# Optimization experiments

Measured on AMD Instinct MI355X. Metric: run time of the kernel, lower is better.

The kernel has to match this reference:

```python
import jax, jax.numpy as jnp
import numpy as np

N = 50000
E = 800000
N_IN = 256
N_HID = 128
N_OUT = 64
HOP = 10


def setup_inputs() -> dict:
    key = jax.random.key(0)
    ks = jax.random.split(key, 12)
    x = jax.random.normal(ks[0], (N, N_IN), dtype=jnp.float32)
    s = jax.random.randint(ks[1], (E,), 0, N, dtype=jnp.int32)
    t = jax.random.randint(ks[2], (E,), 0, N, dtype=jnp.int32)
    # parameters (xavier-ish scaling)
    fc1W = jax.random.normal(ks[3], (N_HID, N_IN), dtype=jnp.float32) * (1.0 / np.sqrt(N_IN))
    fc1b = jnp.zeros((N_HID,), dtype=jnp.float32)
    fcsW = jax.random.normal(ks[4], (HOP, N_HID, N_HID), dtype=jnp.float32) * (1.0 / np.sqrt(N_HID))
    fcsb = jnp.zeros((HOP, N_HID), dtype=jnp.float32)
    a1 = jax.random.normal(ks[5], (HOP, N_HID), dtype=jnp.float32) * (1.0 / np.sqrt(N_HID))
    a2 = jax.random.normal(ks[6], (HOP, N_HID), dtype=jnp.float32) * (1.0 / np.sqrt(N_HID))
    fc2W = jax.random.normal(ks[7], (N_OUT, N_HID), dtype=jnp.float32) * (1.0 / np.sqrt(N_HID))
    fc2b = jnp.zeros((N_OUT,), dtype=jnp.float32)
    return {"x": x, "s": s, "t": t, "fc1W": fc1W, "fc1b": fc1b,
            "fcsW": fcsW, "fcsb": fcsb, "a1": a1, "a2": a2,
            "fc2W": fc2W, "fc2b": fc2b}


def reference(x, s, t, fc1W, fc1b, fcsW, fcsb, a1, a2, fc2W, fc2b):
    # dropout layers are identity in eval mode
    x = jax.nn.relu(x @ fc1W.T + fc1b)  # [N, n_hid]
    h = x
    for i in range(HOP):
        W, b = fcsW[i], fcsb[i]
        x_new = x @ W.T + b          # [N, n_hid]
        h = h @ W.T + b              # [N, n_hid]
        x1 = x_new @ a1[i]           # [N]
        h1 = h @ a2[i]               # [N]
        w1 = jnp.exp(jax.nn.leaky_relu(x1[s] + h1[t], 0.2))       # [E]
        w2 = jnp.exp(jax.nn.leaky_relu(x1 + x_new @ a2[i], 0.2))  # [N]
        div = jax.ops.segment_sum(w1, s, num_segments=N) + w2     # [N]
        num = jax.ops.segment_sum(w1[:, None] * h[t], s, num_segments=N) + w2[:, None] * x_new
        h = jax.nn.elu(num / div[:, None])
    return h @ fc2W.T + fc2b  # [N, n_out]
```

## Files before the change

### kernel.cpp

```cpp
#include <hip/hip_runtime.h>
#include <math.h>


typedef __attribute__((ext_vector_type(8))) short short8;
typedef __attribute__((ext_vector_type(4))) float f32x4;
#define MFMA16 __builtin_amdgcn_mfma_f32_16x16x32_bf16

__device__ __forceinline__ float lrelu02(float v) { return v > 0.f ? v : 0.2f * v; }

__device__ __forceinline__ float2 bf2f2(unsigned int v) {
    return make_float2(__uint_as_float(v << 16), __uint_as_float(v & 0xffff0000u));
}
__device__ __forceinline__ unsigned int f2bf(float f) {
    unsigned int u = __float_as_uint(f);
    u += 0x7fffu + ((u >> 16) & 1u);
    return u >> 16;
}
__device__ __forceinline__ float hi_part(float f) {
    return __uint_as_float(__float_as_uint(f) & 0xffff0000u);
}
__device__ __forceinline__ uint4 pack_hi(const float4& a, const float4& b) {
    uint4 r;
    r.x = (__float_as_uint(a.x) >> 16) | (__float_as_uint(a.y) & 0xffff0000u);
    r.y = (__float_as_uint(a.z) >> 16) | (__float_as_uint(a.w) & 0xffff0000u);
    r.z = (__float_as_uint(b.x) >> 16) | (__float_as_uint(b.y) & 0xffff0000u);
    r.w = (__float_as_uint(b.z) >> 16) | (__float_as_uint(b.w) & 0xffff0000u);
    return r;
}
__device__ __forceinline__ uint4 pack_lo(const float4& a, const float4& b) {
    uint4 r;
    r.x = f2bf(a.x - hi_part(a.x)) | (f2bf(a.y - hi_part(a.y)) << 16);
    r.y = f2bf(a.z - hi_part(a.z)) | (f2bf(a.w - hi_part(a.w)) << 16);
    r.z = f2bf(b.x - hi_part(b.x)) | (f2bf(b.y - hi_part(b.y)) << 16);
    r.w = f2bf(b.z - hi_part(b.z)) | (f2bf(b.w - hi_part(b.w)) << 16);
    return r;
}

__global__ __launch_bounds__(256) void k_count(const int* __restrict__ s, int* __restrict__ cnt, int E) {
    int e = blockIdx.x * 256 + threadIdx.x;
    if (e < E) atomicAdd(&cnt[s[e]], 1);
}

__global__ __launch_bounds__(256) void k_scan1(const int* __restrict__ cnt, int* __restrict__ bs, int N) {
    __shared__ int sh[256];
    int idx = blockIdx.x * 256 + threadIdx.x;
    sh[threadIdx.x] = (idx < N) ? cnt[idx] : 0;
    __syncthreads();
#pragma unroll
    for (int off = 128; off; off >>= 1) {
        if (threadIdx.x < off) sh[threadIdx.x] += sh[threadIdx.x + off];
        __syncthreads();
    }
    if (threadIdx.x == 0) bs[blockIdx.x] = sh[0];
}

__global__ __launch_bounds__(256) void k_scan2(int* __restrict__ bs, int G) {
    __shared__ int sh[256];
    int t = threadIdx.x;
    int v = (t < G) ? bs[t] : 0;
    sh[t] = v;
    __syncthreads();
    int val = v;
#pragma unroll
    for (int off = 1; off < 256; off <<= 1) {
        int o = (t >= off) ? sh[t - off] : 0;
        __syncthreads();
        val += o; sh[t] = val;
        __syncthreads();
    }
    if (t < G) bs[t] = val - v;
}

__global__ __launch_bounds__(256) void k_scan3(const int* __restrict__ cnt, const int* __restrict__ bs,
                                               int* __restrict__ rp, int N) {
    __shared__ int sh[256];
    int t = threadIdx.x;
    int idx = blockIdx.x * 256 + t;
    int v = (idx < N) ? cnt[idx] : 0;
    sh[t] = v;
    __syncthreads();
    int val = v;
#pragma unroll
    for (int off = 1; off < 256; off <<= 1) {
        int o = (t >= off) ? sh[t - off] : 0;
        __syncthreads();
        val += o; sh[t] = val;
        __syncthreads();
    }
    if (idx <= N) rp[idx] = val - v + bs[blockIdx.x];
}

__global__ __launch_bounds__(256) void k_scatter(const int* __restrict__ s, const int* __restrict__ t,
                                                 const int* __restrict__ rp, int* __restrict__ cursor,
                                                 int* __restrict__ t_sorted, int E) {
    int e = blockIdx.x * 256 + threadIdx.x;
    if (e < E) {
        int u = s[e];
        int pos = atomicAdd(&cursor[u], 1);
        t_sorted[rp[u] + pos] = t[e];
    }
}

__global__ __launch_bounds__(256) void k_wsplit(const float* __restrict__ W,
                                                unsigned short* __restrict__ Whi,
                                                unsigned short* __restrict__ Wlo, int total) {
    int i = blockIdx.x * 256 + threadIdx.x;
    if (i < total) {
        float f = W[i];
        unsigned int u = __float_as_uint(f);
        Whi[i] = (unsigned short)(u >> 16);
        Wlo[i] = (unsigned short)f2bf(f - __uint_as_float(u & 0xffff0000u));
    }
}

__global__ __launch_bounds__(256) void k_fc1(
    const float* __restrict__ Xf,
    const unsigned short* __restrict__ Wh, const unsigned short* __restrict__ Wl,
    const float* __restrict__ bias,
    unsigned short* __restrict__ Yhi, unsigned short* __restrict__ Ylo, int N) {
    const int tid = threadIdx.x;
    const int r0 = blockIdx.x * 64;
    const int lane = tid & 63;
    const int w = tid >> 6;
    const int wr = (w >> 1) * 32, wc = (w & 1) * 64;
    const int frow = lane & 15;
    const int fk = lane >> 4;
    const int q4 = lane >> 4;

    f32x4 acc[2][4];
#pragma unroll
    for (int i = 0; i < 2; ++i)
#pragma unroll
        for (int j = 0; j < 4; ++j) acc[i][j] = (f32x4){0.f, 0.f, 0.f, 0.f};

    const float4 z4 = make_float4(0.f, 0.f, 0.f, 0.f);
#pragma unroll
    for (int kc = 0; kc < 8; ++kc) {
        short8 ah[2], al[2];
#pragma unroll
        for (int ri = 0; ri < 2; ++ri) {
            int row = r0 + wr + ri * 16 + frow;
            float4 va = z4, vb = z4;
            if (row < N) {
                const float* p = Xf + (size_t)row * 256 + kc * 32 + fk * 8;
                va = *(const float4*)p;
                vb = *(const float4*)(p + 4);
            }
            uint4 h = pack_hi(va, vb);
            uint4 l = pack_lo(va, vb);
            ah[ri] = *(short8*)&h;
            al[ri] = *(short8*)&l;
        }
#pragma unroll
        for (int ci = 0; ci < 4; ++ci) {
            int col = wc + ci * 16 + frow;
            short8 bh = *(const short8*)(Wh + (size_t)col * 256 + kc * 32 + fk * 8);
            short8 bl = *(const short8*)(Wl + (size_t)col * 256 + kc * 32 + fk * 8);
#pragma unroll
            for (int ri = 0; ri < 2; ++ri) {
                acc[ri][ci] = MFMA16(ah[ri], bh, acc[ri][ci], 0, 0, 0);
                acc[ri][ci] = MFMA16(ah[ri], bl, acc[ri][ci], 0, 0, 0);
                acc[ri][ci] = MFMA16(al[ri], bh, acc[ri][ci], 0, 0, 0);
            }
        }
    }

#pragma unroll
    for (int ci = 0; ci < 4; ++ci) {
        int col = wc + ci * 16 + frow;
        float bcol = bias[col];
#pragma unroll
        for (int ri = 0; ri < 2; ++ri) {
            f32x4 v = acc[ri][ci];
#pragma unroll
            for (int reg = 0; reg < 4; ++reg) {
                int grow = r0 + wr + ri * 16 + q4 * 4 + reg;
                if (grow < N) {
                    float val = fmaxf(v[reg] + bcol, 0.f);
                    Yhi[(size_t)grow * 128 + col] = (unsigned short)(__float_as_uint(val) >> 16);
                    Ylo[(size_t)grow * 128 + col] = (unsigned short)f2bf(val - hi_part(val));
                }
            }
        }
    }
}

__global__ __launch_bounds__(256) void k_fc2(
    const unsigned short* __restrict__ Xhi,
    const unsigned short* __restrict__ Wh, const unsigned short* __restrict__ Wl,
    const float* __restrict__ bias, float* __restrict__ Yf, int N) {
    const int tid = threadIdx.x;
    const int r0 = blockIdx.x * 64;
    const int lane = tid & 63;
    const int w = tid >> 6;
    const int wr = w * 16;
    const int frow = lane & 15;
    const int fk = lane >> 4;
    const int q4 = lane >> 4;

    f32x4 acc[4];
#pragma unroll
    for (int j = 0; j < 4; ++j) acc[j] = (f32x4){0.f, 0.f, 0.f, 0.f};

    const short8 z8 = (short8){0, 0, 0, 0, 0, 0, 0, 0};
#pragma unroll
    for (int kc = 0; kc < 4; ++kc) {
        int row = r0 + wr + frow;
        short8 ah = (row < N) ? *(const short8*)(Xhi + (size_t)row * 128 + kc * 32 + fk * 8) : z8;
#pragma unroll
        for (int ci = 0; ci < 4; ++ci) {
            int col = ci * 16 + frow;
            short8 bh = *(const short8*)(Wh + (size_t)col * 128 + kc * 32 + fk * 8);
            short8 bl = *(const short8*)(Wl + (size_t)col * 128 + kc * 32 + fk * 8);
            acc[ci] = MFMA16(ah, bh, acc[ci], 0, 0, 0);
            acc[ci] = MFMA16(ah, bl, acc[ci], 0, 0, 0);
        }
    }

#pragma unroll
    for (int ci = 0; ci < 4; ++ci) {
        int col = ci * 16 + frow;
        float bcol = bias[col];
#pragma unroll
        for (int reg = 0; reg < 4; ++reg) {
            int grow = r0 + wr + q4 * 4 + reg;
            if (grow < N) Yf[(size_t)grow * 64 + col] = acc[ci][reg] + bcol;
        }
    }
}

__global__ __launch_bounds__(256) void k_xall(
    const unsigned short* __restrict__ Xhi, const unsigned short* __restrict__ Xlo, int NB,
    const unsigned short* __restrict__ Whi_all, const unsigned short* __restrict__ Wlo_all,
    const float* __restrict__ fcsb, const float* __restrict__ a1, const float* __restrict__ a2,
    int i0, unsigned short* __restrict__ xnb_all,
    float* __restrict__ x1a_all, float* __restrict__ xa2a_all, int N) {
    __shared__ unsigned short lds[2 * 128 * 128];

    const int tid = threadIdx.x;
    const int islot = (int)blockIdx.x / NB;
    const int bx = (int)blockIdx.x % NB;
    const int ih = i0 + islot;
    const unsigned short* Wh = Whi_all + (size_t)ih * 16384;
    const unsigned short* Wl = Wlo_all + (size_t)ih * 16384;
    const float* bias = fcsb + ih * 128;
    const float* dA = a1 + ih * 128;
    const float* dB = a2 + ih * 128;
    unsigned short* Yb = xnb_all + (size_t)islot * N * 128;
    float* oA = x1a_all + (size_t)islot * N;
    float* oB = xa2a_all + (size_t)islot * N;
    const int r0 = bx * 128;

    {
        int col = tid & 127;
        int pl = tid >> 7;
        const unsigned short* wp = (pl ? Wl : Wh) + (size_t)col * 128;
        unsigned short* dst = lds + pl * 16384 + col * 128;
#pragma unroll
        for (int g = 0; g < 16; ++g)
            *(uint4*)(dst + ((g ^ (col & 7)) * 8)) = ((const uint4*)wp)[g];
    }
    __syncthreads();

    const int lane = tid & 63;
    const int w = tid >> 6;
    const int wr = (w >> 1) * 64, wc = (w & 1) * 64;
    const int frow = lane & 15;
    const int fk = lane >> 4;
    const int q4 = lane >> 4;

    f32x4 acc[4][4];
#pragma unroll
    for (int i = 0; i < 4; ++i)
#pragma unroll
        for (int j = 0; j < 4; ++j) acc[i][j] = (f32x4){0.f, 0.f, 0.f, 0.f};

    const short8 z8 = (short8){0, 0, 0, 0, 0, 0, 0, 0};

#pragma unroll
    for (int kc = 0; kc < 4; ++kc) {
        short8 ah[4], al[4], bh[4], bl[4];
#pragma unroll
        for (int ri = 0; ri < 4; ++ri) {
            int row = r0 + wr + ri * 16 + frow;
            bool ok = row < N;
            ah[ri] = ok ? *(const short8*)(Xhi + (size_t)row * 128 + kc * 32 + fk * 8) : z8;
            al[ri] = ok ? *(const short8*)(Xlo + (size_t)row * 128 + kc * 32 + fk * 8) : z8;
        }
#pragma unroll
        for (int ci = 0; ci < 4; ++ci) {
            int col = wc + ci * 16 + frow;
            int g = kc * 4 + fk;
            int go = (g ^ (col & 7)) * 8;
            bh[ci] = *(const short8*)(lds + col * 128 + go);
            bl[ci] = *(const short8*)(lds + 16384 + col * 128 + go);
        }
#pragma unroll
        for (int ri = 0; ri < 4; ++ri)
#pragma unroll
            for (int ci = 0; ci < 4; ++ci) {
                acc[ri][ci] = MFMA16(ah[ri], bh[ci], acc[ri][ci], 0, 0, 0);
                acc[ri][ci] = MFMA16(ah[ri], bl[ci], acc[ri][ci], 0, 0, 0);
                acc[ri][ci] = MFMA16(al[ri], bh[ci], acc[ri][ci], 0, 0, 0);
            }
    }

    unsigned short* So = lds;
    float* dotbuf = (float*)(lds + 16384);

    float dotA[4][4] = {}, dotB[4][4] = {};
    __syncthreads();
#pragma unroll
    for (int ci = 0; ci < 4; ++ci) {
        int col = wc + ci * 16 + frow;
        float bcol = bias[col];
        float dAc = dA[col];
        float dBc = dB[col];
#pragma unroll
        for (int ri = 0; ri < 4; ++ri) {
            f32x4 v = acc[ri][ci];
#pragma unroll
            for (int reg = 0; reg < 4; ++reg) {
                float val = v[reg] + bcol;
                int row = wr + ri * 16 + q4 * 4 + reg;
                int dw = (col >> 1) ^ ((row & 12) << 1);
                So[row * 128 + dw * 2 + (col & 1)] = (unsigned short)f2bf(val);
                dotA[ri][reg] = fmaf(val, dAc, dotA[ri][reg]);
                dotB[ri][reg] = fmaf(val, dBc, dotB[ri][reg]);
            }
        }
    }
#pragma unroll
    for (int m = 1; m < 16; m <<= 1)
#pragma unroll
        for (int ri = 0; ri < 4; ++ri)
#pragma unroll
            for (int reg = 0; reg < 4; ++reg) {
                dotA[ri][reg] += __shfl_xor(dotA[ri][reg], m, 64);
                dotB[ri][reg] += __shfl_xor(dotB[ri][reg], m, 64);
            }
    if (frow == 0) {
#pragma unroll
        for (int ri = 0; ri < 4; ++ri)
#pragma unroll
            for (int reg = 0; reg < 4; ++reg) {
                int rl = wr + ri * 16 + q4 * 4 + reg;
                dotbuf[(0 * 128 + rl) * 2 + (w & 1)] = dotA[ri][reg];
                dotbuf[(1 * 128 + rl) * 2 + (w & 1)] = dotB[ri][reg];
            }
    }
    __syncthreads();

#pragma unroll
    for (int q = 0; q < 8; ++q) {
        int idx = q * 256 + tid;
        int row = idx >> 4;
        int gc = idx & 15;
        int dwb = (gc * 4) ^ ((row & 12) << 1);
        uint4 vv = *(const uint4*)(So + row * 128 + dwb * 2);
        int grow = r0 + row;
        if (grow < N) *(uint4*)(Yb + (size_t)grow * 128 + gc * 8) = vv;
    }
    {
        int d = tid >> 7, rl = tid & 127;
        int grow = r0 + rl;
        if (grow < N) {
            float v = dotbuf[(d * 128 + rl) * 2] + dotbuf[(d * 128 + rl) * 2 + 1];
            if (d == 0) oA[grow] = v;
            else        oB[grow] = v;
        }
    }
}

__global__ __launch_bounds__(256) void k_hh(
    const unsigned short* __restrict__ Hhi,
    const unsigned short* __restrict__ Wh, const unsigned short* __restrict__ Wl,
    const float* __restrict__ bias, const float* __restrict__ dA2,
    unsigned short* __restrict__ hbf, float* __restrict__ h1a, int N) {
    __shared__ unsigned short So[64 * 128];
    __shared__ float dotbuf[64][2];
    const int tid = threadIdx.x;
    const int r0 = blockIdx.x * 64;
    const int lane = tid & 63;
    const int w = tid >> 6;
    const int wr = (w >> 1) * 32, wc = (w & 1) * 64;
    const int frow = lane & 15;
    const int fk = lane >> 4;
    const int q4 = lane >> 4;

    f32x4 acc[2][4];
#pragma unroll
    for (int i = 0; i < 2; ++i)
#pragma unroll
        for (int j = 0; j < 4; ++j) acc[i][j] = (f32x4){0.f, 0.f, 0.f, 0.f};

    const short8 z8 = (short8){0, 0, 0, 0, 0, 0, 0, 0};
#pragma unroll
    for (int kc = 0; kc < 4; ++kc) {
        short8 ah[2];
#pragma unroll
        for (int ri = 0; ri < 2; ++ri) {
            int row = r0 + wr + ri * 16 + frow;
            ah[ri] = (row < N) ? *(const short8*)(Hhi + (size_t)row * 128 + kc * 32 + fk * 8) : z8;
        }
#pragma unroll
        for (int ci = 0; ci < 4; ++ci) {
            int col = wc + ci * 16 + frow;
            short8 bh = *(const short8*)(Wh + (size_t)col * 128 + kc * 32 + fk * 8);
            short8 bl = *(const short8*)(Wl + (size_t)col * 128 + kc * 32 + fk * 8);
#pragma unroll
            for (int ri = 0; ri < 2; ++ri) {
                acc[ri][ci] = MFMA16(ah[ri], bh, acc[ri][ci], 0, 0, 0);
                acc[ri][ci] = MFMA16(ah[ri], bl, acc[ri][ci], 0, 0, 0);
            }
        }
    }

    float dotA[2][4] = {};
#pragma unroll
    for (int ci = 0; ci < 4; ++ci) {
        int col = wc + ci * 16 + frow;
        float bcol = bias[col];
        float dAc = dA2[col];
#pragma unroll
        for (int ri = 0; ri < 2; ++ri) {
            f32x4 v = acc[ri][ci];
#pragma unroll
            for (int reg = 0; reg < 4; ++reg) {
                float val = v[reg] + bcol;
                int row = wr + ri * 16 + q4 * 4 + reg;
                int dw = (col >> 1) ^ ((row & 12) << 1);
                So[row * 128 + dw * 2 + (col & 1)] = (unsigned short)f2bf(val);
                dotA[ri][reg] = fmaf(val, dAc, dotA[ri][reg]);
            }
        }
    }
#pragma unroll
    for (int m = 1; m < 16; m <<= 1)
#pragma unroll
        for (int ri = 0; ri < 2; ++ri)
#pragma unroll
            for (int reg = 0; reg < 4; ++reg)
                dotA[ri][reg] += __shfl_xor(dotA[ri][reg], m, 64);
    if (frow == 0) {
#pragma unroll
        for (int ri = 0; ri < 2; ++ri)
#pragma unroll
            for (int reg = 0; reg < 4; ++reg) {
                int rl = wr + ri * 16 + q4 * 4 + reg;
                dotbuf[rl][w & 1] = dotA[ri][reg];
            }
    }
    __syncthreads();

#pragma unroll
    for (int q = 0; q < 4; ++q) {
        int idx = q * 256 + tid;
        int row = idx >> 4;
        int gc = idx & 15;
        int dwb = (gc * 4) ^ ((row & 12) << 1);
        uint4 vv = *(const uint4*)(So + row * 128 + dwb * 2);
        int grow = r0 + row;
        if (grow < N) *(uint4*)(hbf + (size_t)grow * 128 + gc * 8) = vv;
    }
    if (tid < 64) {
        int grow = r0 + tid;
        if (grow < N) h1a[grow] = dotbuf[tid][0] + dotbuf[tid][1];
    }
}

__global__ __launch_bounds__(256) void k_agg(
    const unsigned short* __restrict__ xnb, const unsigned short* __restrict__ hbf,
    const float* __restrict__ x1a, const float* __restrict__ xa2a,
    const float* __restrict__ h1a, const int* __restrict__ rp,
    const int* __restrict__ ts,
    unsigned short* __restrict__ hhi, int N) {
    __shared__ uint2 ew[4][64];
    const int wid = threadIdx.x >> 6;
    const int lane = threadIdx.x & 63;
    const int u = blockIdx.x * 4 + wid;
    if (u >= N) return;
    const int l2 = lane << 1;
    float x1u = x1a[u];
    float w2 = expf(lrelu02(x1u + xa2a[u]));
    float2 xr = bf2f2(*(const unsigned int*)(xnb + (size_t)u * 128 + l2));
    float accx = w2 * xr.x, accy = w2 * xr.y;
    float div = w2;
    int p0 = rp[u], p1 = rp[u + 1];
    for (int base = p0; base < p1; base += 64) {
        int e = base + lane;
        uint2 pk = make_uint2(0u, 0u);
        if (e < p1) {
            int tv = ts[e];
            pk.x = (unsigned int)tv;
            pk.y = __float_as_uint(expf(lrelu02(x1u + h1a[tv])));
        }
        ew[wid][lane] = pk;
        int m = p1 - base; if (m > 64) m = 64;
        int m8 = (m + 7) & ~7;
        for (int j = 0; j < m8; j += 8) {
            uint2 q[8];
#pragma unroll
            for (int k = 0; k < 8; ++k) q[k] = ew[wid][j + k];
            unsigned int hv[8];
#pragma unroll
            for (int k = 0; k < 8; ++k)
                hv[k] = *(const unsigned int*)(hbf + (size_t)q[k].x * 128 + l2);
#pragma unroll
            for (int k = 0; k < 8; ++k) {
                float ww = __uint_as_float(q[k].y);
                float2 f = bf2f2(hv[k]);
                accx = fmaf(ww, f.x, accx);
                accy = fmaf(ww, f.y, accy);
                div += ww;
            }
        }
    }
    float ox = accx / div, oy = accy / div;
    ox = ox > 0.f ? ox : expf(ox) - 1.f;
    oy = oy > 0.f ? oy : expf(oy) - 1.f;
    unsigned int hx = __float_as_uint(ox), hy = __float_as_uint(oy);
    *(unsigned int*)(hhi + (size_t)u * 128 + l2) = (hx >> 16) | (hy & 0xffff0000u);
}

extern "C" void kernel_launch(void* const* d_in, const int* in_sizes, int n_in,
                              void* d_out, int out_size, void* d_ws, size_t ws_size,
                              hipStream_t stream) {
    const float* x_in = (const float*)d_in[0];
    const int*   s    = (const int*)d_in[1];
    const int*   t    = (const int*)d_in[2];
    const float* fc1W = (const float*)d_in[3];
    const float* fc1b = (const float*)d_in[4];
    const float* fcsW = (const float*)d_in[5];
    const float* fcsb = (const float*)d_in[6];
    const float* a1   = (const float*)d_in[7];
    const float* a2   = (const float*)d_in[8];
    const float* fc2W = (const float*)d_in[9];
    const float* fc2b = (const float*)d_in[10];

    const int N = in_sizes[0] / 256;
    const int E = in_sizes[1];
    const int G = (N + 255) / 256;
    const int NB = (N + 127) / 128;
    const int NB64 = (N + 63) / 64;

    auto A256 = [](size_t b) { return (b + 255) & ~(size_t)255; };
    const size_t plane = A256((size_t)N * 128 * 2);
    const size_t vecN  = A256((size_t)N * 4);
    size_t fixed = 3 * plane
                 + plane
                 + 2 * A256((size_t)10 * 16384 * 2)
                 + 2 * A256((size_t)128 * 256 * 2) + 2 * A256((size_t)64 * 128 * 2)
                 + vecN
                 + A256((size_t)(N + 1) * 4) + vecN + A256(1024) + A256((size_t)E * 4);
    const int BATCH = (fixed + 10 * (plane + 2 * vecN) <= ws_size) ? 10 : 1;

    char* ws = (char*)d_ws;
    size_t off = 0;
    auto alloc = [&](size_t bytes) -> void* {
        void* p = ws + off;
        off += (bytes + 255) & ~(size_t)255;
        return p;
    };
    unsigned short* xbuf_hi = (unsigned short*)alloc((size_t)N * 128 * 2);
    unsigned short* xbuf_lo = (unsigned short*)alloc((size_t)N * 128 * 2);
    unsigned short* h_hi    = (unsigned short*)alloc((size_t)N * 128 * 2);
    unsigned short* hbf     = (unsigned short*)alloc((size_t)N * 128 * 2);
    unsigned short* Whi  = (unsigned short*)alloc((size_t)10 * 16384 * 2);
    unsigned short* Wlo  = (unsigned short*)alloc((size_t)10 * 16384 * 2);
    unsigned short* W1hi = (unsigned short*)alloc((size_t)128 * 256 * 2);
    unsigned short* W1lo = (unsigned short*)alloc((size_t)128 * 256 * 2);
    unsigned short* W2hi = (unsigned short*)alloc((size_t)64 * 128 * 2);
    unsigned short* W2lo = (unsigned short*)alloc((size_t)64 * 128 * 2);
    float* h1a  = (float*)alloc((size_t)N * 4);
    int* row_ptr  = (int*)alloc((size_t)(N + 1) * 4);
    int* cnt      = (int*)alloc((size_t)N * 4);
    int* bsums    = (int*)alloc((size_t)1024);
    int* t_sorted = (int*)alloc((size_t)E * 4);
    unsigned short* xnb_all = (unsigned short*)alloc((size_t)BATCH * N * 128 * 2);
    float* x1a_all  = (float*)alloc((size_t)BATCH * N * 4);
    float* xa2a_all = (float*)alloc((size_t)BATCH * N * 4);

    hipMemsetAsync(cnt, 0, (size_t)N * 4, stream);
    k_count<<<(E + 255) / 256, 256, 0, stream>>>(s, cnt, E);
    k_scan1<<<G, 256, 0, stream>>>(cnt, bsums, N);
    k_scan2<<<1, 256, 0, stream>>>(bsums, G);
    k_scan3<<<G, 256, 0, stream>>>(cnt, bsums, row_ptr, N);
    hipMemsetAsync(cnt, 0, (size_t)N * 4, stream);
    k_scatter<<<(E + 255) / 256, 256, 0, stream>>>(s, t, row_ptr, cnt, t_sorted, E);

    k_wsplit<<<(10 * 16384 + 255) / 256, 256, 0, stream>>>(fcsW, Whi, Wlo, 10 * 16384);
    k_wsplit<<<(128 * 256 + 255) / 256, 256, 0, stream>>>(fc1W, W1hi, W1lo, 128 * 256);
    k_wsplit<<<(64 * 128 + 255) / 256, 256, 0, stream>>>(fc2W, W2hi, W2lo, 64 * 128);

    k_fc1<<<NB64, 256, 0, stream>>>(x_in, W1hi, W1lo, fc1b, xbuf_hi, xbuf_lo, N);

    if (BATCH == 10)
        k_xall<<<10 * NB, 256, 0, stream>>>(xbuf_hi, xbuf_lo, NB, Whi, Wlo,
                                            fcsb, a1, a2, 0, xnb_all, x1a_all, xa2a_all, N);

    for (int i = 0; i < 10; ++i) {
        if (BATCH == 1)
            k_xall<<<NB, 256, 0, stream>>>(xbuf_hi, xbuf_lo, NB, Whi, Wlo,
                                           fcsb, a1, a2, i, xnb_all, x1a_all, xa2a_all, N);
        const int sl = (BATCH == 10) ? i : 0;
        const unsigned short* xnb_i = xnb_all + (size_t)sl * N * 128;
        const float* x1_i  = x1a_all + (size_t)sl * N;
        const float* xa2_i = xa2a_all + (size_t)sl * N;
        if (i == 0) {
            k_agg<<<(N + 3) / 4, 256, 0, stream>>>(xnb_i, xnb_i, x1_i, xa2_i, xa2_i,
                                                   row_ptr, t_sorted, h_hi, N);
        } else {
            k_hh<<<NB64, 256, 0, stream>>>(h_hi, Whi + (size_t)i * 16384, Wlo + (size_t)i * 16384,
                                           fcsb + (size_t)i * 128, a2 + (size_t)i * 128,
                                           hbf, h1a, N);
            k_agg<<<(N + 3) / 4, 256, 0, stream>>>(xnb_i, hbf, x1_i, xa2_i, h1a,
                                                   row_ptr, t_sorted, h_hi, N);
        }
    }

    k_fc2<<<NB64, 256, 0, stream>>>(h_hi, W2hi, W2lo, fc2b, (float*)d_out, N);
}
```

Before: 851.6 us.

## Aggregate before the per-hop linear layer and precompute attention projection vectors

Uses linearity of the per-hop linear layer. Neighbours' un-transformed features are aggregated first, then one GEMM (with ELU fused) is applied to the aggregate. This removes the ten full x_new GEMMs and their large bf16 output planes. The attention scalars x1, x·a2 and h·a2 come from precomputed vectors W^T·a and constants b·a: one small MFMA pass for all hops, plus a fused dot in the GEMM epilogue. The trade-off is bf16 rounding of the aggregate before the GEMM, and a reordered summation that may change numerics slightly.

```diff
diff --git a/kernel.cpp b/kernel.cpp
--- a/kernel.cpp
+++ b/kernel.cpp
@@ -110,6 +110,38 @@
         unsigned int u = __float_as_uint(f);
         Whi[i] = (unsigned short)(u >> 16);
         Wlo[i] = (unsigned short)f2bf(f - __uint_as_float(u & 0xffff0000u));
+    }
+}
+
+__global__ __launch_bounds__(256) void k_prep(
+    const float* __restrict__ fcsW, const float* __restrict__ fcsb,
+    const float* __restrict__ a1, const float* __restrict__ a2,
+    float* __restrict__ Vf, unsigned short* __restrict__ Vh,
+    unsigned short* __restrict__ Vl, float* __restrict__ cvec) {
+    int i = blockIdx.x;
+    int t = threadIdx.x;
+    const float* W = fcsW + (size_t)i * 16384;
+    if (t < 128) {
+        float s1 = 0.f, s2 = 0.f;
+        for (int j = 0; j < 128; ++j) {
+            float w = W[j * 128 + t];
+            s1 = fmaf(w, a1[i * 128 + j], s1);
+            s2 = fmaf(w, a2[i * 128 + j], s2);
+        }
+        Vf[i * 128 + t] = s1;
+        Vf[(16 + i) * 128 + t] = s2;
+        Vh[i * 128 + t] = (unsigned short)(__float_as_uint(s1) >> 16);
+        Vl[i * 128 + t] = (unsigned short)f2bf(s1 - hi_part(s1));
+        Vh[(16 + i) * 128 + t] = (unsigned short)(__float_as_uint(s2) >> 16);
+        Vl[(16 + i) * 128 + t] = (unsigned short)f2bf(s2 - hi_part(s2));
+    } else if (t == 128) {
+        float c1 = 0.f, c2 = 0.f;
+        for (int j = 0; j < 128; ++j) {
+            c1 = fmaf(fcsb[i * 128 + j], a1[i * 128 + j], c1);
+            c2 = fmaf(fcsb[i * 128 + j], a2[i * 128 + j], c2);
+        }
+        cvec[i] = c1;
+        cvec[16 + i] = c2;
     }
 }
 
@@ -185,6 +217,212 @@
     }
 }
 
+__global__ __launch_bounds__(256) void k_xdots(
+    const unsigned short* __restrict__ Xhi, const unsigned short* __restrict__ Xlo,
+    const unsigned short* __restrict__ Vh, const unsigned short* __restrict__ Vl,
+    const float* __restrict__ cvec,
+    float* __restrict__ x1a_all, float* __restrict__ xa2a_all, int N) {
+    const int tid = threadIdx.x;
+    const int r0 = blockIdx.x * 64;
+    const int lane = tid & 63;
+    const int w = tid >> 6;
+    const int wr = w * 16;
+    const int frow = lane & 15;
+    const int fk = lane >> 4;
+    const int q4 = lane >> 4;
+
+    f32x4 acc[2];
+    acc[0] = (f32x4){0.f, 0.f, 0.f, 0.f};
+    acc[1] = (f32x4){0.f, 0.f, 0.f, 0.f};
+
+    const short8 z8 = (short8){0, 0, 0, 0, 0, 0, 0, 0};
+#pragma unroll
+    for (int kc = 0; kc < 4; ++kc) {
+        int row = r0 + wr + frow;
+        bool ok = row < N;
+        short8 ah = ok ? *(const short8*)(Xhi + (size_t)row * 128 + kc * 32 + fk * 8) : z8;
+        short8 al = ok ? *(const short8*)(Xlo + (size_t)row * 128 + kc * 32 + fk * 8) : z8;
+#pragma unroll
+        for (int ci = 0; ci < 2; ++ci) {
+            int col = ci * 16 + frow;
+            short8 bh = *(const short8*)(Vh + (size_t)col * 128 + kc * 32 + fk * 8);
+            short8 bl = *(const short8*)(Vl + (size_t)col * 128 + kc * 32 + fk * 8);
+            acc[ci] = MFMA16(ah, bh, acc[ci], 0, 0, 0);
+            acc[ci] = MFMA16(ah, bl, acc[ci], 0, 0, 0);
+            acc[ci] = MFMA16(al, bh, acc[ci], 0, 0, 0);
+        }
+    }
+
+#pragma unroll
+    for (int ci = 0; ci < 2; ++ci) {
+        int col = ci * 16 + frow;
+        float c = cvec[col];
+#pragma unroll
+        for (int reg = 0; reg < 4; ++reg) {
+            int grow = r0 + wr + q4 * 4 + reg;
+            if (grow < N) {
+                float val = acc[ci][reg] + c;
+                if (col < 10) x1a_all[(size_t)col * N + grow] = val;
+                else if (col >= 16 && col < 26) xa2a_all[(size_t)(col - 16) * N + grow] = val;
+            }
+        }
+    }
+}
+
+__global__ __launch_bounds__(256) void k_gemm(
+    const unsigned short* __restrict__ G,
+    const unsigned short* __restrict__ Wh, const unsigned short* __restrict__ Wl,
+    const float* __restrict__ bias, const float* __restrict__ vnext,
+    const float* __restrict__ cnextp,
+    unsigned short* __restrict__ Hout, float* __restrict__ h1a, int N) {
+    __shared__ unsigned short So[64 * 128];
+    __shared__ float dotbuf[64][2];
+    const int tid = threadIdx.x;
+    const int r0 = blockIdx.x * 64;
+    const int lane = tid & 63;
+    const int w = tid >> 6;
+    const int wr = (w >> 1) * 32, wc = (w & 1) * 64;
+    const int frow = lane & 15;
+    const int fk = lane >> 4;
+    const int q4 = lane >> 4;
+    const bool dodot = vnext != nullptr;
+
+    f32x4 acc[2][4];
+#pragma unroll
+    for (int i = 0; i < 2; ++i)
+#pragma unroll
+        for (int j = 0; j < 4; ++j) acc[i][j] = (f32x4){0.f, 0.f, 0.f, 0.f};
+
+    const short8 z8 = (short8){0, 0, 0, 0, 0, 0, 0, 0};
+#pragma unroll
+    for (int kc = 0; kc < 4; ++kc) {
+        short8 ah[2];
+#pragma unroll
+        for (int ri = 0; ri < 2; ++ri) {
+            int row = r0 + wr + ri * 16 + frow;
+            ah[ri] = (row < N) ? *(const short8*)(G + (size_t)row * 128 + kc * 32 + fk * 8) : z8;
+        }
+#pragma unroll
+        for (int ci = 0; ci < 4; ++ci) {
+            int col = wc + ci * 16 + frow;
+            short8 bh = *(const short8*)(Wh + (size_t)col * 128 + kc * 32 + fk * 8);
+            short8 bl = *(const short8*)(Wl + (size_t)col * 128 + kc * 32 + fk * 8);
+#pragma unroll
+            for (int ri = 0; ri < 2; ++ri) {
+                acc[ri][ci] = MFMA16(ah[ri], bh, acc[ri][ci], 0, 0, 0);
+                acc[ri][ci] = MFMA16(ah[ri], bl, acc[ri][ci], 0, 0, 0);
+            }
+        }
+    }
+
+    float dotA[2][4] = {};
+#pragma unroll
+    for (int ci = 0; ci < 4; ++ci) {
+        int col = wc + ci * 16 + frow;
+        float bcol = bias[col];
+        float vc = dodot ? vnext[col] : 0.f;
+#pragma unroll
+        for (int ri = 0; ri < 2; ++ri) {
+            f32x4 v = acc[ri][ci];
+#pragma unroll
+            for (int reg = 0; reg < 4; ++reg) {
+                float val = v[reg] + bcol;
+                val = val > 0.f ? val : expf(val) - 1.f;
+                int row = wr + ri * 16 + q4 * 4 + reg;
+                int dw = (col >> 1) ^ ((row & 12) << 1);
+                So[row * 128 + dw * 2 + (col & 1)] = (unsigned short)f2bf(val);
+                dotA[ri][reg] = fmaf(val, vc, dotA[ri][reg]);
+            }
+        }
+    }
+#pragma unroll
+    for (int m = 1; m < 16; m <<= 1)
+#pragma unroll
+        for (int ri = 0; ri < 2; ++ri)
+#pragma unroll
+            for (int reg = 0; reg < 4; ++reg)
+                dotA[ri][reg] += __shfl_xor(dotA[ri][reg], m, 64);
+    if (frow == 0) {
+#pragma unroll
+        for (int ri = 0; ri < 2; ++ri)
+#pragma unroll
+            for (int reg = 0; reg < 4; ++reg) {
+                int rl = wr + ri * 16 + q4 * 4 + reg;
+                dotbuf[rl][w & 1] = dotA[ri][reg];
+            }
+    }
+    __syncthreads();
+
+#pragma unroll
+    for (int q = 0; q < 4; ++q) {
+        int idx = q * 256 + tid;
+        int row = idx >> 4;
+        int gc = idx & 15;
+        int dwb = (gc * 4) ^ ((row & 12) << 1);
+        uint4 vv = *(const uint4*)(So + row * 128 + dwb * 2);
+        int grow = r0 + row;
+        if (grow < N) *(uint4*)(Hout + (size_t)grow * 128 + gc * 8) = vv;
+    }
+    if (dodot && tid < 64) {
+        int grow = r0 + tid;
+        if (grow < N) h1a[grow] = dotbuf[tid][0] + dotbuf[tid][1] + cnextp[0];
+    }
+}
+
+__global__ __launch_bounds__(256) void k_agg(
+    const unsigned short* __restrict__ xh, const unsigned short* __restrict__ xl,
+    const unsigned short* __restrict__ table,
+    const float* __restrict__ x1a, const float* __restrict__ xa2a,
+    const float* __restrict__ h1a, const int* __restrict__ rp,
+    const int* __restrict__ ts,
+    unsigned short* __restrict__ g_out, int N) {
+    __shared__ uint2 ew[4][64];
+    const int wid = threadIdx.x >> 6;
+    const int lane = threadIdx.x & 63;
+    const int u = blockIdx.x * 4 + wid;
+    if (u >= N) return;
+    const int l2 = lane << 1;
+    float x1u = x1a[u];
+    float w2 = expf(lrelu02(x1u + xa2a[u]));
+    unsigned int sh = *(const unsigned int*)(xh + (size_t)u * 128 + l2);
+    unsigned int sl = *(const unsigned int*)(xl + (size_t)u * 128 + l2);
+    float2 hx = bf2f2(sh), lx = bf2f2(sl);
+    float accx = w2 * (hx.x + lx.x), accy = w2 * (hx.y + lx.y);
+    float div = w2;
+    int p0 = rp[u], p1 = rp[u + 1];
+    for (int base = p0; base < p1; base += 64) {
+        int e = base + lane;
+        uint2 pk = make_uint2(0u, 0u);
+        if (e < p1) {
+            int tv = ts[e];
+            pk.x = (unsigned int)tv;
+            pk.y = __float_as_uint(expf(lrelu02(x1u + h1a[tv])));
+        }
+        ew[wid][lane] = pk;
+        int m = p1 - base; if (m > 64) m = 64;
+        int m8 = (m + 7) & ~7;
+        for (int j = 0; j < m8; j += 8) {
+            uint2 q[8];
+#pragma unroll
+            for (int k = 0; k < 8; ++k) q[k] = ew[wid][j + k];
+            unsigned int hv[8];
+#pragma unroll
+            for (int k = 0; k < 8; ++k)
+                hv[k] = *(const unsigned int*)(table + (size_t)q[k].x * 128 + l2);
+#pragma unroll
+            for (int k = 0; k < 8; ++k) {
+                float ww = __uint_as_float(q[k].y);
+                float2 f = bf2f2(hv[k]);
+                accx = fmaf(ww, f.x, accx);
+                accy = fmaf(ww, f.y, accy);
+                div += ww;
+            }
+        }
+    }
+    float ox = accx / div, oy = accy / div;
+    *(unsigned int*)(g_out + (size_t)u * 128 + l2) = f2bf(ox) | (f2bf(oy) << 16);
+}
+
 __global__ __launch_bounds__(256) void k_fc2(
     const unsigned short* __restrict__ Xhi,
     const unsigned short* __restrict__ Wh, const unsigned short* __restrict__ Wl,
@@ -227,300 +465,6 @@
             if (grow < N) Yf[(size_t)grow * 64 + col] = acc[ci][reg] + bcol;
         }
     }
-}
-
-__global__ __launch_bounds__(256) void k_xall(
-    const unsigned short* __restrict__ Xhi, const unsigned short* __restrict__ Xlo, int NB,
-    const unsigned short* __restrict__ Whi_all, const unsigned short* __restrict__ Wlo_all,
-    const float* __restrict__ fcsb, const float* __restrict__ a1, const float* __restrict__ a2,
-    int i0, unsigned short* __restrict__ xnb_all,
-    float* __restrict__ x1a_all, float* __restrict__ xa2a_all, int N) {
-    __shared__ unsigned short lds[2 * 128 * 128];
-
-    const int tid = threadIdx.x;
-    const int islot = (int)blockIdx.x / NB;
-    const int bx = (int)blockIdx.x % NB;
-    const int ih = i0 + islot;
-    const unsigned short* Wh = Whi_all + (size_t)ih * 16384;
-    const unsigned short* Wl = Wlo_all + (size_t)ih * 16384;
-    const float* bias = fcsb + ih * 128;
-    const float* dA = a1 + ih * 128;
-    const float* dB = a2 + ih * 128;
-    unsigned short* Yb = xnb_all + (size_t)islot * N * 128;
-    float* oA = x1a_all + (size_t)islot * N;
-    float* oB = xa2a_all + (size_t)islot * N;
-    const int r0 = bx * 128;
-
-    {
-        int col = tid & 127;
-        int pl = tid >> 7;
-        const unsigned short* wp = (pl ? Wl : Wh) + (size_t)col * 128;
-        unsigned short* dst = lds + pl * 16384 + col * 128;
-#pragma unroll
-        for (int g = 0; g < 16; ++g)
-            *(uint4*)(dst + ((g ^ (col & 7)) * 8)) = ((const uint4*)wp)[g];
-    }
-    __syncthreads();
-
-    const int lane = tid & 63;
-    const int w = tid >> 6;
-    const int wr = (w >> 1) * 64, wc = (w & 1) * 64;
-    const int frow = lane & 15;
-    const int fk = lane >> 4;
-    const int q4 = lane >> 4;
-
-    f32x4 acc[4][4];
-#pragma unroll
-    for (int i = 0; i < 4; ++i)
-#pragma unroll
-        for (int j = 0; j < 4; ++j) acc[i][j] = (f32x4){0.f, 0.f, 0.f, 0.f};
-
-    const short8 z8 = (short8){0, 0, 0, 0, 0, 0, 0, 0};
-
-#pragma unroll
-    for (int kc = 0; kc < 4; ++kc) {
-        short8 ah[4], al[4], bh[4], bl[4];
-#pragma unroll
-        for (int ri = 0; ri < 4; ++ri) {
-            int row = r0 + wr + ri * 16 + frow;
-            bool ok = row < N;
-            ah[ri] = ok ? *(const short8*)(Xhi + (size_t)row * 128 + kc * 32 + fk * 8) : z8;
-            al[ri] = ok ? *(const short8*)(Xlo + (size_t)row * 128 + kc * 32 + fk * 8) : z8;
-        }
-#pragma unroll
-        for (int ci = 0; ci < 4; ++ci) {
-            int col = wc + ci * 16 + frow;
-            int g = kc * 4 + fk;
-            int go = (g ^ (col & 7)) * 8;
-            bh[ci] = *(const short8*)(lds + col * 128 + go);
-            bl[ci] = *(const short8*)(lds + 16384 + col * 128 + go);
-        }
-#pragma unroll
-        for (int ri = 0; ri < 4; ++ri)
-#pragma unroll
-            for (int ci = 0; ci < 4; ++ci) {
-                acc[ri][ci] = MFMA16(ah[ri], bh[ci], acc[ri][ci], 0, 0, 0);
-                acc[ri][ci] = MFMA16(ah[ri], bl[ci], acc[ri][ci], 0, 0, 0);
-                acc[ri][ci] = MFMA16(al[ri], bh[ci], acc[ri][ci], 0, 0, 0);
-            }
-    }
-
-    unsigned short* So = lds;
-    float* dotbuf = (float*)(lds + 16384);
-
-    float dotA[4][4] = {}, dotB[4][4] = {};
-    __syncthreads();
-#pragma unroll
-    for (int ci = 0; ci < 4; ++ci) {
-        int col = wc + ci * 16 + frow;
-        float bcol = bias[col];
-        float dAc = dA[col];
-        float dBc = dB[col];
-#pragma unroll
-        for (int ri = 0; ri < 4; ++ri) {
-            f32x4 v = acc[ri][ci];
-#pragma unroll
-            for (int reg = 0; reg < 4; ++reg) {
-                float val = v[reg] + bcol;
-                int row = wr + ri * 16 + q4 * 4 + reg;
-                int dw = (col >> 1) ^ ((row & 12) << 1);
-                So[row * 128 + dw * 2 + (col & 1)] = (unsigned short)f2bf(val);
-                dotA[ri][reg] = fmaf(val, dAc, dotA[ri][reg]);
-                dotB[ri][reg] = fmaf(val, dBc, dotB[ri][reg]);
-            }
-        }
-    }
-#pragma unroll
-    for (int m = 1; m < 16; m <<= 1)
-#pragma unroll
-        for (int ri = 0; ri < 4; ++ri)
-#pragma unroll
-            for (int reg = 0; reg < 4; ++reg) {
-                dotA[ri][reg] += __shfl_xor(dotA[ri][reg], m, 64);
-                dotB[ri][reg] += __shfl_xor(dotB[ri][reg], m, 64);
-            }
-    if (frow == 0) {
-#pragma unroll
-        for (int ri = 0; ri < 4; ++ri)
-#pragma unroll
-            for (int reg = 0; reg < 4; ++reg) {
-                int rl = wr + ri * 16 + q4 * 4 + reg;
-                dotbuf[(0 * 128 + rl) * 2 + (w & 1)] = dotA[ri][reg];
-                dotbuf[(1 * 128 + rl) * 2 + (w & 1)] = dotB[ri][reg];
-            }
-    }
-    __syncthreads();
-
-#pragma unroll
-    for (int q = 0; q < 8; ++q) {
-        int idx = q * 256 + tid;
-        int row = idx >> 4;
-        int gc = idx & 15;
-        int dwb = (gc * 4) ^ ((row & 12) << 1);
-        uint4 vv = *(const uint4*)(So + row * 128 + dwb * 2);
-        int grow = r0 + row;
-        if (grow < N) *(uint4*)(Yb + (size_t)grow * 128 + gc * 8) = vv;
-    }
-    {
-        int d = tid >> 7, rl = tid & 127;
-        int grow = r0 + rl;
-        if (grow < N) {
-            float v = dotbuf[(d * 128 + rl) * 2] + dotbuf[(d * 128 + rl) * 2 + 1];
-            if (d == 0) oA[grow] = v;
-            else        oB[grow] = v;
-        }
-    }
-}
-
-__global__ __launch_bounds__(256) void k_hh(
-    const unsigned short* __restrict__ Hhi,
-    const unsigned short* __restrict__ Wh, const unsigned short* __restrict__ Wl,
-    const float* __restrict__ bias, const float* __restrict__ dA2,
-    unsigned short* __restrict__ hbf, float* __restrict__ h1a, int N) {
-    __shared__ unsigned short So[64 * 128];
-    __shared__ float dotbuf[64][2];
-    const int tid = threadIdx.x;
-    const int r0 = blockIdx.x * 64;
-    const int lane = tid & 63;
-    const int w = tid >> 6;
-    const int wr = (w >> 1) * 32, wc = (w & 1) * 64;
-    const int frow = lane & 15;
-    const int fk = lane >> 4;
-    const int q4 = lane >> 4;
-
-    f32x4 acc[2][4];
-#pragma unroll
-    for (int i = 0; i < 2; ++i)
-#pragma unroll
-        for (int j = 0; j < 4; ++j) acc[i][j] = (f32x4){0.f, 0.f, 0.f, 0.f};
-
-    const short8 z8 = (short8){0, 0, 0, 0, 0, 0, 0, 0};
-#pragma unroll
-    for (int kc = 0; kc < 4; ++kc) {
-        short8 ah[2];
-#pragma unroll
-        for (int ri = 0; ri < 2; ++ri) {
-            int row = r0 + wr + ri * 16 + frow;
-            ah[ri] = (row < N) ? *(const short8*)(Hhi + (size_t)row * 128 + kc * 32 + fk * 8) : z8;
-        }
-#pragma unroll
-        for (int ci = 0; ci < 4; ++ci) {
-            int col = wc + ci * 16 + frow;
-            short8 bh = *(const short8*)(Wh + (size_t)col * 128 + kc * 32 + fk * 8);
-            short8 bl = *(const short8*)(Wl + (size_t)col * 128 + kc * 32 + fk * 8);
-#pragma unroll
-            for (int ri = 0; ri < 2; ++ri) {
-                acc[ri][ci] = MFMA16(ah[ri], bh, acc[ri][ci], 0, 0, 0);
-                acc[ri][ci] = MFMA16(ah[ri], bl, acc[ri][ci], 0, 0, 0);
-            }
-        }
-    }
-
-    float dotA[2][4] = {};
-#pragma unroll
-    for (int ci = 0; ci < 4; ++ci) {
-        int col = wc + ci * 16 + frow;
-        float bcol = bias[col];
-        float dAc = dA2[col];
-#pragma unroll
-        for (int ri = 0; ri < 2; ++ri) {
-            f32x4 v = acc[ri][ci];
-#pragma unroll
-            for (int reg = 0; reg < 4; ++reg) {
-                float val = v[reg] + bcol;
-                int row = wr + ri * 16 + q4 * 4 + reg;
-                int dw = (col >> 1) ^ ((row & 12) << 1);
-                So[row * 128 + dw * 2 + (col & 1)] = (unsigned short)f2bf(val);
-                dotA[ri][reg] = fmaf(val, dAc, dotA[ri][reg]);
-            }
-        }
-    }
-#pragma unroll
-    for (int m = 1; m < 16; m <<= 1)
-#pragma unroll
-        for (int ri = 0; ri < 2; ++ri)
-#pragma unroll
-            for (int reg = 0; reg < 4; ++reg)
-                dotA[ri][reg] += __shfl_xor(dotA[ri][reg], m, 64);
-    if (frow == 0) {
-#pragma unroll
-        for (int ri = 0; ri < 2; ++ri)
-#pragma unroll
-            for (int reg = 0; reg < 4; ++reg) {
-                int rl = wr + ri * 16 + q4 * 4 + reg;
-                dotbuf[rl][w & 1] = dotA[ri][reg];
-            }
-    }
-    __syncthreads();
-
-#pragma unroll
-    for (int q = 0; q < 4; ++q) {
-        int idx = q * 256 + tid;
-        int row = idx >> 4;
-        int gc = idx & 15;
-        int dwb = (gc * 4) ^ ((row & 12) << 1);
-        uint4 vv = *(const uint4*)(So + row * 128 + dwb * 2);
-        int grow = r0 + row;
-        if (grow < N) *(uint4*)(hbf + (size_t)grow * 128 + gc * 8) = vv;
-    }
-    if (tid < 64) {
-        int grow = r0 + tid;
-        if (grow < N) h1a[grow] = dotbuf[tid][0] + dotbuf[tid][1];
-    }
-}
-
-__global__ __launch_bounds__(256) void k_agg(
-    const unsigned short* __restrict__ xnb, const unsigned short* __restrict__ hbf,
-    const float* __restrict__ x1a, const float* __restrict__ xa2a,
-    const float* __restrict__ h1a, const int* __restrict__ rp,
-    const int* __restrict__ ts,
-    unsigned short* __restrict__ hhi, int N) {
-    __shared__ uint2 ew[4][64];
-    const int wid = threadIdx.x >> 6;
-    const int lane = threadIdx.x & 63;
-    const int u = blockIdx.x * 4 + wid;
-    if (u >= N) return;
-    const int l2 = lane << 1;
-    float x1u = x1a[u];
-    float w2 = expf(lrelu02(x1u + xa2a[u]));
-    float2 xr = bf2f2(*(const unsigned int*)(xnb + (size_t)u * 128 + l2));
-    float accx = w2 * xr.x, accy = w2 * xr.y;
-    float div = w2;
-    int p0 = rp[u], p1 = rp[u + 1];
-    for (int base = p0; base < p1; base += 64) {
-        int e = base + lane;
-        uint2 pk = make_uint2(0u, 0u);
-        if (e < p1) {
-            int tv = ts[e];
-            pk.x = (unsigned int)tv;
-            pk.y = __float_as_uint(expf(lrelu02(x1u + h1a[tv])));
-        }
-        ew[wid][lane] = pk;
-        int m = p1 - base; if (m > 64) m = 64;
-        int m8 = (m + 7) & ~7;
-        for (int j = 0; j < m8; j += 8) {
-            uint2 q[8];
-#pragma unroll
-            for (int k = 0; k < 8; ++k) q[k] = ew[wid][j + k];
-            unsigned int hv[8];
-#pragma unroll
-            for (int k = 0; k < 8; ++k)
-                hv[k] = *(const unsigned int*)(hbf + (size_t)q[k].x * 128 + l2);
-#pragma unroll
-            for (int k = 0; k < 8; ++k) {
-                float ww = __uint_as_float(q[k].y);
-                float2 f = bf2f2(hv[k]);
-                accx = fmaf(ww, f.x, accx);
-                accy = fmaf(ww, f.y, accy);
-                div += ww;
-            }
-        }
-    }
-    float ox = accx / div, oy = accy / div;
-    ox = ox > 0.f ? ox : expf(ox) - 1.f;
-    oy = oy > 0.f ? oy : expf(oy) - 1.f;
-    unsigned int hx = __float_as_uint(ox), hy = __float_as_uint(oy);
-    *(unsigned int*)(hhi + (size_t)u * 128 + l2) = (hx >> 16) | (hy & 0xffff0000u);
 }
 
 extern "C" void kernel_launch(void* const* d_in, const int* in_sizes, int n_in,
@@ -541,19 +485,7 @@
     const int N = in_sizes[0] / 256;
     const int E = in_sizes[1];
     const int G = (N + 255) / 256;
-    const int NB = (N + 127) / 128;
     const int NB64 = (N + 63) / 64;
-
-    auto A256 = [](size_t b) { return (b + 255) & ~(size_t)255; };
-    const size_t plane = A256((size_t)N * 128 * 2);
-    const size_t vecN  = A256((size_t)N * 4);
-    size_t fixed = 3 * plane
-                 + plane
-                 + 2 * A256((size_t)10 * 16384 * 2)
-                 + 2 * A256((size_t)128 * 256 * 2) + 2 * A256((size_t)64 * 128 * 2)
-                 + vecN
-                 + A256((size_t)(N + 1) * 4) + vecN + A256(1024) + A256((size_t)E * 4);
-    const int BATCH = (fixed + 10 * (plane + 2 * vecN) <= ws_size) ? 10 : 1;
 
     char* ws = (char*)d_ws;
     size_t off = 0;
@@ -565,21 +497,24 @@
     unsigned short* xbuf_hi = (unsigned short*)alloc((size_t)N * 128 * 2);
     unsigned short* xbuf_lo = (unsigned short*)alloc((size_t)N * 128 * 2);
     unsigned short* h_hi    = (unsigned short*)alloc((size_t)N * 128 * 2);
-    unsigned short* hbf     = (unsigned short*)alloc((size_t)N * 128 * 2);
+    unsigned short* gbuf    = (unsigned short*)alloc((size_t)N * 128 * 2);
     unsigned short* Whi  = (unsigned short*)alloc((size_t)10 * 16384 * 2);
     unsigned short* Wlo  = (unsigned short*)alloc((size_t)10 * 16384 * 2);
     unsigned short* W1hi = (unsigned short*)alloc((size_t)128 * 256 * 2);
     unsigned short* W1lo = (unsigned short*)alloc((size_t)128 * 256 * 2);
     unsigned short* W2hi = (unsigned short*)alloc((size_t)64 * 128 * 2);
     unsigned short* W2lo = (unsigned short*)alloc((size_t)64 * 128 * 2);
+    float* Vf   = (float*)alloc((size_t)32 * 128 * 4);
+    unsigned short* Vh = (unsigned short*)alloc((size_t)32 * 128 * 2);
+    unsigned short* Vl = (unsigned short*)alloc((size_t)32 * 128 * 2);
+    float* cvec = (float*)alloc((size_t)32 * 4);
+    float* x1a_all  = (float*)alloc((size_t)10 * N * 4);
+    float* xa2a_all = (float*)alloc((size_t)10 * N * 4);
     float* h1a  = (float*)alloc((size_t)N * 4);
     int* row_ptr  = (int*)alloc((size_t)(N + 1) * 4);
     int* cnt      = (int*)alloc((size_t)N * 4);
     int* bsums    = (int*)alloc((size_t)1024);
     int* t_sorted = (int*)alloc((size_t)E * 4);
-    unsigned short* xnb_all = (unsigned short*)alloc((size_t)BATCH * N * 128 * 2);
-    float* x1a_all  = (float*)alloc((size_t)BATCH * N * 4);
-    float* xa2a_all = (float*)alloc((size_t)BATCH * N * 4);
 
     hipMemsetAsync(cnt, 0, (size_t)N * 4, stream);
     k_count<<<(E + 255) / 256, 256, 0, stream>>>(s, cnt, E);
@@ -592,31 +527,30 @@
     k_wsplit<<<(10 * 16384 + 255) / 256, 256, 0, stream>>>(fcsW, Whi, Wlo, 10 * 16384);
     k_wsplit<<<(128 * 256 + 255) / 256, 256, 0, stream>>>(fc1W, W1hi, W1lo, 128 * 256);
     k_wsplit<<<(64 * 128 + 255) / 256, 256, 0, stream>>>(fc2W, W2hi, W2lo, 64 * 128);
+    hipMemsetAsync(Vf, 0, (size_t)32 * 128 * 4, stream);
+    hipMemsetAsync(Vh, 0, (size_t)32 * 128 * 2, stream);
+    hipMemsetAsync(Vl, 0, (size_t)32 * 128 * 2, stream);
+    hipMemsetAsync(cvec, 0, (size_t)32 * 4, stream);
+    k_prep<<<10, 256, 0, stream>>>(fcsW, fcsb, a1, a2, Vf, Vh, Vl, cvec);
 
     k_fc1<<<NB64, 256, 0, stream>>>(x_in, W1hi, W1lo, fc1b, xbuf_hi, xbuf_lo, N);
 
-    if (BATCH == 10)
-        k_xall<<<10 * NB, 256, 0, stream>>>(xbuf_hi, xbuf_lo, NB, Whi, Wlo,
-                                            fcsb, a1, a2, 0, xnb_all, x1a_all, xa2a_all, N);
+    k_xdots<<<NB64, 256, 0, stream>>>(xbuf_hi, xbuf_lo, Vh, Vl, cvec,
+                                      x1a_all, xa2a_all, N);
 
     for (int i = 0; i < 10; ++i) {
-        if (BATCH == 1)
-            k_xall<<<NB, 256, 0, stream>>>(xbuf_hi, xbuf_lo, NB, Whi, Wlo,
-                                           fcsb, a1, a2, i, xnb_all, x1a_all, xa2a_all, N);
-        const int sl = (BATCH == 10) ? i : 0;
-        const unsigned short* xnb_i = xnb_all + (size_t)sl * N * 128;
-        const float* x1_i  = x1a_all + (size_t)sl * N;
-        const float* xa2_i = xa2a_all + (size_t)sl * N;
-        if (i == 0) {
-            k_agg<<<(N + 3) / 4, 256, 0, stream>>>(xnb_i, xnb_i, x1_i, xa2_i, xa2_i,
-                                                   row_ptr, t_sorted, h_hi, N);
-        } else {
-            k_hh<<<NB64, 256, 0, stream>>>(h_hi, Whi + (size_t)i * 16384, Wlo + (size_t)i * 16384,
-                                           fcsb + (size_t)i * 128, a2 + (size_t)i * 128,
-                                           hbf, h1a, N);
-            k_agg<<<(N + 3) / 4, 256, 0, stream>>>(xnb_i, hbf, x1_i, xa2_i, h1a,
-                                                   row_ptr, t_sorted, h_hi, N);
-        }
+        const unsigned short* table = (i == 0) ? xbuf_hi : h_hi;
+        const float* h1_i = (i == 0) ? (xa2a_all + 0) : h1a;
+        k_agg<<<(N + 3) / 4, 256, 0, stream>>>(xbuf_hi, xbuf_lo, table,
+                                               x1a_all + (size_t)i * N,
+                                               xa2a_all + (size_t)i * N,
+                                               h1_i, row_ptr, t_sorted, gbuf, N);
+        const float* vnext = (i < 9) ? (Vf + (size_t)(16 + i + 1) * 128) : nullptr;
+        const float* cnextp = cvec + (16 + i + 1);
+        k_gemm<<<NB64, 256, 0, stream>>>(gbuf, Whi + (size_t)i * 16384,
+                                         Wlo + (size_t)i * 16384,
+                                         fcsb + (size_t)i * 128, vnext, cnextp,
+                                         h_hi, h1a, N);
     }
 
     k_fc2<<<NB64, 256, 0, stream>>>(h_hi, W2hi, W2lo, fc2b, (float*)d_out, N);
```

After: 806.3 us. 5.3% less time.
